# Optimization experiments

Hardware: AMD Instinct MI355X
Metric: run time of the kernel (lower is better)

The kernel has to match this reference:

```python
import jax, jax.numpy as jnp
import numpy as np

B, S, T, E, H = 64, 128, 128, 512, 1024
NEG = -1e9


def setup_inputs() -> dict:
    key = jax.random.key(0)
    ks = jax.random.split(key, 11)
    sc = 0.05
    return {
        "inputs": jax.random.normal(ks[0], (B, T, E), jnp.float32),
        "encoder_hiddens": jax.random.normal(ks[1], (B, S, H), jnp.float32),
        "encoder_finals": jax.random.normal(ks[2], (1, B, H), jnp.float32),
        "src_mask": jnp.ones((B, S), dtype=bool),
        # Bahdanau attention params (torch nn.Linear convention: y = x @ W.T)
        "W_key": jax.random.normal(ks[3], (H, H), jnp.float32) * sc,
        "W_query": jax.random.normal(ks[4], (H, H), jnp.float32) * sc,
        "v_att": jax.random.normal(ks[5], (H,), jnp.float32) * sc,
        # single-layer GRU params, torch gate order (r, z, n)
        "W_ih": jax.random.normal(ks[6], (3 * H, E + H), jnp.float32) * sc,
        "W_hh": jax.random.normal(ks[7], (3 * H, H), jnp.float32) * sc,
        "b_ih": jax.random.normal(ks[8], (3 * H,), jnp.float32) * sc,
        "b_hh": jax.random.normal(ks[9], (3 * H,), jnp.float32) * sc,
    }


def reference(inputs, encoder_hiddens, encoder_finals, src_mask,
              W_key, W_query, v_att, W_ih, W_hh, b_ih, b_hh):
    h_dim = encoder_hiddens.shape[-1]
    # proj_key computed once outside the loop, as in the original
    proj_key = jnp.einsum('bsh,kh->bsk', encoder_hiddens, W_key)  # (B,S,H)

    def step(hidden, x_t):
        # hidden: (1,B,H); x_t: (B,E)
        h = hidden[-1]                                  # (B,H)
        q = h @ W_query.T                               # (B,H)
        e = jnp.tanh(q[:, None, :] + proj_key) @ v_att  # (B,S)
        e = jnp.where(src_mask, e, NEG)
        alphas = jax.nn.softmax(e, axis=-1)
        ctx = jnp.einsum('bs,bsh->bh', alphas, encoder_hiddens)  # (B,H)
        x = jnp.concatenate([x_t, ctx], axis=-1)        # (B,E+H)
        gx = x @ W_ih.T + b_ih                          # (B,3H)
        gh = h @ W_hh.T + b_hh                          # (B,3H)
        r = jax.nn.sigmoid(gx[:, :h_dim] + gh[:, :h_dim])
        z = jax.nn.sigmoid(gx[:, h_dim:2 * h_dim] + gh[:, h_dim:2 * h_dim])
        n = jnp.tanh(gx[:, 2 * h_dim:] + r * gh[:, 2 * h_dim:])
        h_new = (1.0 - z) * n + z * h
        return h_new[None], h_new

    hidden, outs = jax.lax.scan(step, encoder_finals, jnp.swapaxes(inputs, 0, 1))
    outputs = jnp.swapaxes(outs, 0, 1)  # (B,T,H)
    return hidden, outputs
```

## Files before the change

kernel.cpp:

```cpp
#include <hip/hip_runtime.h>
#include <hip/hip_cooperative_groups.h>

namespace cg = cooperative_groups;

#define Bb 64
#define Ss 128
#define Tt 128
#define Ee 512
#define Hh 1024
#define GRID 256
#define NTHR 512
#define GSTRIDE (GRID * NTHR)

using short8 = __attribute__((ext_vector_type(8))) short;
using f32x4  = __attribute__((ext_vector_type(4))) float;
typedef unsigned long long u64;

#define PK_OFF    0u
#define EPART_OFF PK_OFF
#define ENC_OFF   16777216u
#define WQF_OFF   33554432u
#define WHHF_OFF  35651584u
#define WIHF_OFF  41943040u
#define WKF_OFF   51380224u
#define QWS_OFF   53477376u
#define GHWS_OFF  53739520u
#define CTXF_OFF  54525952u
#define HFRG_OFF  54657024u
#define HPRV_OFF  54788096u
#define FLG_OFF   55050240u

__device__ __forceinline__ float fast_tanh(float x) {
  float e = __expf(2.0f * x);
  return 1.0f - __fdividef(2.0f, e + 1.0f);
}
__device__ __forceinline__ float fast_sig(float x) {
  return __fdividef(1.0f, 1.0f + __expf(-x));
}
__device__ __forceinline__ unsigned f2bf(float x) {
  union { float f; unsigned u; } v; v.f = x;
  unsigned r = v.u + 0x7fffu + ((v.u >> 16) & 1u);
  return (r >> 16);
}
__device__ __forceinline__ uint4 pack8(float4 a, float4 b) {
  uint4 u;
  u.x = f2bf(a.x) | (f2bf(a.y) << 16);
  u.y = f2bf(a.z) | (f2bf(a.w) << 16);
  u.z = f2bf(b.x) | (f2bf(b.y) << 16);
  u.w = f2bf(b.z) | (f2bf(b.w) << 16);
  return u;
}
__device__ __forceinline__ void cvt8_store(const float* src, unsigned short* dst) {
  float4 f0 = *(const float4*)src, f1 = *(const float4*)(src + 4);
  *(uint4*)dst = pack8(f0, f1);
}
__device__ __forceinline__ short8 ld_frag(const unsigned short* base, int tile, int lane) {
  return *(const short8*)(base + ((size_t)tile * 64 + lane) * 8);
}
__device__ __forceinline__ short8 cvt8_reg(const float* src) {
  float4 f0 = *(const float4*)src, f1 = *(const float4*)(src + 4);
  union { uint4 u; short8 s; } cv; cv.u = pack8(f0, f1);
  return cv.s;
}

__device__ __forceinline__ u64 ld_coh8(const void* p) {
  return __hip_atomic_load((const u64*)p, __ATOMIC_RELAXED, __HIP_MEMORY_SCOPE_AGENT);
}
__device__ __forceinline__ void st_coh8(void* p, u64 v) {
  __hip_atomic_store((u64*)p, v, __ATOMIC_RELAXED, __HIP_MEMORY_SCOPE_AGENT);
}
__device__ __forceinline__ unsigned ld_coh1(const void* p) {
  return __hip_atomic_load((const unsigned*)p, __ATOMIC_RELAXED, __HIP_MEMORY_SCOPE_AGENT);
}
__device__ __forceinline__ void st_coh1(void* p, unsigned v) {
  __hip_atomic_store((unsigned*)p, v, __ATOMIC_RELAXED, __HIP_MEMORY_SCOPE_AGENT);
}
__device__ __forceinline__ void add_coh1(void* p, unsigned v) {
  __hip_atomic_fetch_add((unsigned*)p, v, __ATOMIC_RELAXED, __HIP_MEMORY_SCOPE_AGENT);
}
__device__ __forceinline__ u64 f2u64(float a, float b) {
  union { float f[2]; u64 u; } c; c.f[0] = a; c.f[1] = b; return c.u;
}
__device__ __forceinline__ float u64lo(u64 v) {
  union { unsigned u; float f; } c; c.u = (unsigned)v; return c.f;
}
__device__ __forceinline__ float u64hi(u64 v) {
  union { unsigned u; float f; } c; c.u = (unsigned)(v >> 32); return c.f;
}

#define ARRIVE_PRE() do { \
  asm volatile("s_waitcnt vmcnt(0)" ::: "memory"); \
  __syncthreads(); } while (0)

template <int K, bool PERM>
__device__ void conv_frag(const float* __restrict__ W, unsigned short* __restrict__ F,
                          int gtid, int total) {
  const int kpg = K / 8;
  for (int i = gtid; i < total; i += GSTRIDE) {
    int np = i / kpg, kg = i - np * kpg;
    int row;
    if (PERM) {
      int ntp = np >> 4, jb = ntp / 3, g = ntp - jb * 3;
      row = g * 1024 + jb * 16 + (np & 15);
    } else row = np;
    int k0 = kg * 8;
    int kt = k0 >> 5, quad = (k0 >> 3) & 3;
    int lane_f = (np & 15) | (quad << 4);
    size_t dst = ((size_t)((np >> 4) * (K / 32) + kt) * 64 + lane_f) * 8;
    cvt8_store(W + (size_t)row * K + k0, F + dst);
  }
}

__global__ void __launch_bounds__(NTHR, 2)
bahdanau_kernel(const float* __restrict__ inputs,
                const float* __restrict__ enc,
                const float* __restrict__ finals,
                const float* __restrict__ Wk,
                const float* __restrict__ Wq,
                const float* __restrict__ vatt,
                const float* __restrict__ Wih,
                const float* __restrict__ Whh,
                const float* __restrict__ bih,
                const float* __restrict__ bhh,
                float* __restrict__ dout,
                char* __restrict__ wsb)
{
  cg::grid_group grid = cg::this_grid();
  __shared__ unsigned short pk_l[128][256];
  __shared__ char scr[40960];

  const int tid  = threadIdx.x;
  const int bid  = blockIdx.x;
  const int lane = tid & 63;
  const int wv   = __builtin_amdgcn_readfirstlane(tid >> 6);
  const int gtid = bid * NTHR + tid;
  const int quad = lane >> 4, col = lane & 15;

  unsigned short* pk   = (unsigned short*)(wsb + PK_OFF);
  float*          epart= (float*)(wsb + EPART_OFF);
  unsigned short* encb = (unsigned short*)(wsb + ENC_OFF);
  unsigned short* wqf  = (unsigned short*)(wsb + WQF_OFF);
  unsigned short* wihf = (unsigned short*)(wsb + WIHF_OFF);
  unsigned short* wkf  = (unsigned short*)(wsb + WKF_OFF);
  float* qws  = (float*)(wsb + QWS_OFF);
  float* ghws = (float*)(wsb + GHWS_OFF);
  unsigned short* ctxf = (unsigned short*)(wsb + CTXF_OFF);
  unsigned short* hfrg = (unsigned short*)(wsb + HFRG_OFF);
  float* hprv = (float*)(wsb + HPRV_OFF);
  unsigned* flags = (unsigned*)(wsb + FLG_OFF);
  unsigned* af = flags;
  unsigned* mb = flags + 8192;
  unsigned* cc = flags + 10240;
  unsigned* hc = flags + 12288;
  unsigned* rc = flags + 13312;
  unsigned* ha = flags + 14336;
  float* hidout = dout;
  float* outs   = dout + Bb * Hh;

  const int batt = bid & 63;
  const int hq   = bid >> 6;

  for (int i = gtid; i < 16384; i += GSTRIDE) flags[i] = 0u;
  for (int i = gtid; i < 1048576; i += GSTRIDE)
    cvt8_store(enc + (size_t)i * 8, encb + (size_t)i * 8);
  conv_frag<1024, false>(Wq,  wqf,  gtid, 131072);
  conv_frag<1024, false>(Wk,  wkf,  gtid, 131072);
  conv_frag<1024, true >(Whh, (unsigned short*)(wsb + WHHF_OFF), gtid, 393216);
  conv_frag<1536, true >(Wih, wihf, gtid, 589824);
  for (int i = gtid; i < 8192; i += GSTRIDE) {
    int b = i >> 7, kg = i & 127, k0 = kg * 8;
    int kt = k0 >> 5, qd = (k0 >> 3) & 3;
    int lf = (b & 15) | (qd << 4);
    cvt8_store(finals + (size_t)b * Hh + k0,
               hfrg + ((size_t)((b >> 4) * 32 + kt) * 64 + lf) * 8);
  }
  for (int i = gtid; i < 16384; i += GSTRIDE)
    ((float4*)hprv)[i] = ((const float4*)finals)[i];
  grid.sync();

  const int wA  = (bid & 7) * 8 + (bid >> 5);
  const int btA = (bid >> 3) & 3;
  const int cgA = wv & 3;
  const int khA = wv >> 2;
  const int ntA = wA * 4 + cgA;
  short8 wAB[16];
  #pragma unroll
  for (int i = 0; i < 16; ++i)
    wAB[i] = ld_frag(wqf, ntA * 32 + khA * 16 + i, lane);

  const int cxC = bid & 7, cmC = bid >> 3;
  const int jbC = cxC * 8 + (cmC >> 2);
  const int bqC = cmC & 3;

  int pqsel;
  {
    int g = lane & 3;
    int wq = hq * 4 + g;
    pqsel = (wq & 7) * 32 + (batt >> 4) * 8 + (wq >> 3);
  }
  int pghsel;
  {
    int wg0 = (64 + 3 * jbC) >> 2, wg1 = (66 + 3 * jbC) >> 2;
    int wg = (lane == 16) ? wg0 : wg1;
    pghsel = (wg & 7) * 32 + bqC * 8 + (wg >> 3);
  }

  float vr2[4];
  {
    float4 vv = *(const float4*)(vatt + hq * 256 + lane * 4);
    vr2[0] = vv.x; vr2[1] = vv.y; vr2[2] = vv.z; vr2[3] = vv.w;
  }

  {
    const int W = bid * 8 + wv;
    const int mt = W >> 2;
    const int ng = W & 3;
    for (int nt2 = 0; nt2 < 16; ++nt2) {
      int nt = ng * 16 + nt2;
      f32x4 acc = {0.f, 0.f, 0.f, 0.f};
      for (int kt = 0; kt < 32; ++kt) {
        short8 a = *(const short8*)(encb + (size_t)(mt * 16 + col) * Hh + kt * 32 + quad * 8);
        short8 b = ld_frag(wkf, nt * 32 + kt, lane);
        acc = __builtin_amdgcn_mfma_f32_16x16x32_bf16(a, b, acc, 0, 0, 0);
      }
      #pragma unroll
      for (int r = 0; r < 4; ++r)
        pk[(size_t)(mt * 16 + quad * 4 + r) * Hh + nt * 16 + col] = (unsigned short)f2bf(acc[r]);
    }
  }
  grid.sync();

  {
    const unsigned short* src = pk + (size_t)batt * Ss * Hh + hq * 256;
    int s = tid >> 2, pq = tid & 3;
    #pragma unroll
    for (int i = 0; i < 8; ++i)
      *(uint4*)&pk_l[s][pq * 64 + i * 8] =
        *(const uint4*)(src + (size_t)s * Hh + pq * 64 + i * 8);
  }
  __syncthreads();

  for (int t = 0; t < Tt; ++t) {
    const unsigned genA = (unsigned)(t + 1);

    __syncthreads();
    if (t > 0 && tid < 64) {
      unsigned tgt = 8u * (unsigned)t;
      for (;;) {
        bool ok = true;
        if (lane < 8) ok = ld_coh1(&hc[(btA * 8 + lane) * 32]) >= tgt;
        if (__all(ok)) break;
        __builtin_amdgcn_s_sleep(2);
      }
    }
    __syncthreads();

    {
      {
        u64* l8 = (u64*)scr;
        const u64* g8 = (const u64*)(hfrg + (size_t)btA * 32 * 64 * 8);
        u64 r[8];
        #pragma unroll
        for (int i = 0; i < 8; ++i) r[i] = ld_coh8(g8 + tid + i * NTHR);
        #pragma unroll
        for (int i = 0; i < 8; ++i) l8[tid + i * NTHR] = r[i];
      }
      __syncthreads();
      if (tid == 0) add_coh1(&ha[(btA * 8 + (wA >> 3)) * 32], 1u);
      const unsigned short* hl = (const unsigned short*)scr;
      f32x4 acc = {0.f, 0.f, 0.f, 0.f};
      #pragma unroll
      for (int i = 0; i < 16; ++i) {
        int kt = khA * 16 + i;
        short8 a = *(const short8*)(hl + ((size_t)kt * 64 + lane) * 8);
        acc = __builtin_amdgcn_mfma_f32_16x16x32_bf16(a, wAB[i], acc, 0, 0, 0);
      }
      __syncthreads();
      float* part = (float*)(scr + 32768);
      #pragma unroll
      for (int r = 0; r < 4; ++r) part[r * 512 + wv * 64 + lane] = acc[r];
      __syncthreads();
      {
        int cg = tid >> 7, rem = tid & 127;
        int qd = rem >> 5, r = (rem >> 3) & 3, clp = rem & 7;
        float v2[2];
        #pragma unroll
        for (int jj = 0; jj < 2; ++jj) {
          int cl = clp * 2 + jj;
          int ln = (qd << 4) | cl;
          v2[jj] = part[r * 512 + cg * 64 + ln]
                 + part[r * 512 + (4 + cg) * 64 + ln];
        }
        int b = btA * 16 + qd * 4 + r;
        int nt_g = wA * 4 + cg;
        if (nt_g < 64)
          st_coh8(&qws[(size_t)b * Hh + nt_g * 16 + clp * 2], f2u64(v2[0], v2[1]));
        else
          st_coh8(&ghws[((size_t)(nt_g - 64) * 64 + b) * 16 + clp * 2], f2u64(v2[0], v2[1]));
      }
    }
    ARRIVE_PRE();
    if (tid == 0) st_coh1(&af[bid * 32], genA);

    if (tid < 64) {
      for (;;) {
        bool ok = true;
        if (lane < 4) ok = ld_coh1(&af[pqsel * 32]) >= genA;
        if (__all(ok)) break;
        __builtin_amdgcn_s_sleep(2);
      }
    }
    __syncthreads();

    {
      float* ep_s = (float*)scr;
      float qr2[4];
      {
        const u64* qb = (const u64*)(qws + (size_t)batt * Hh + hq * 256);
        u64 q01 = ld_coh8(qb + lane * 2), q23 = ld_coh8(qb + lane * 2 + 1);
        qr2[0] = u64lo(q01); qr2[1] = u64hi(q01);
        qr2[2] = u64lo(q23); qr2[3] = u64hi(q23);
      }
      for (int si = 0; si < 16; ++si) {
        int s = wv * 16 + si;
        u64 pkv = *(const u64*)&pk_l[s][lane << 2];
        float pv0 = __uint_as_float(((unsigned)pkv & 0xffffu) << 16);
        float pv1 = __uint_as_float((unsigned)pkv & 0xffff0000u);
        float pv2 = __uint_as_float(((unsigned)(pkv >> 32) & 0xffffu) << 16);
        float pv3 = __uint_as_float((unsigned)(pkv >> 32) & 0xffff0000u);
        float p = vr2[0] * fast_tanh(qr2[0] + pv0);
        p = fmaf(vr2[1], fast_tanh(qr2[1] + pv1), p);
        p = fmaf(vr2[2], fast_tanh(qr2[2] + pv2), p);
        p = fmaf(vr2[3], fast_tanh(qr2[3] + pv3), p);
        #pragma unroll
        for (int m = 1; m < 64; m <<= 1) p += __shfl_xor(p, m, 64);
        if (lane == 0) ep_s[s] = p;
      }
      __syncthreads();
      if (tid < 64) {
        float2 e2 = *(const float2*)&ep_s[tid * 2];
        st_coh8(&epart[((size_t)batt * 4 + hq) * 128 + tid * 2], f2u64(e2.x, e2.y));
      }
    }
    ARRIVE_PRE();
    if (tid == 0) add_coh1(&mb[batt * 32], 1u);
    if (tid == 0) {
      while (ld_coh1(&mb[batt * 32]) < 4u * genA) __builtin_amdgcn_s_sleep(2);
    }
    __syncthreads();

    {
      float* e_s  = (float*)(scr + 512);
      float* al_s = (float*)(scr + 1024);
      float* comb = (float*)(scr + 1536);
      if (tid < 64) {
        float s0 = 0.f, s1 = 0.f;
        #pragma unroll
        for (int k = 0; k < 4; ++k) {
          u64 v = ld_coh8(&epart[((size_t)batt * 4 + k) * 128 + tid * 2]);
          s0 += u64lo(v); s1 += u64hi(v);
        }
        e_s[tid * 2] = s0; e_s[tid * 2 + 1] = s1;
      }
      __syncthreads();
      if (wv == 0) {
        float x0 = e_s[lane], x1 = e_s[lane + 64];
        float m = fmaxf(x0, x1);
        #pragma unroll
        for (int mm = 1; mm < 64; mm <<= 1) m = fmaxf(m, __shfl_xor(m, mm, 64));
        float ex0 = __expf(x0 - m), ex1 = __expf(x1 - m);
        float ssum = ex0 + ex1;
        #pragma unroll
        for (int mm = 1; mm < 64; mm <<= 1) ssum += __shfl_xor(ssum, mm, 64);
        float inv = __fdividef(1.0f, ssum);
        al_s[lane] = ex0 * inv; al_s[lane + 64] = ex1 * inv;
      }
      __syncthreads();
      {
        int tq = tid >> 7, hh = tid & 127;
        float c0 = 0.f, c1 = 0.f;
        const unsigned short* ebase = encb + ((size_t)batt * Ss + tq * 32) * Hh
                                    + hq * 256 + hh * 2;
        #pragma unroll 8
        for (int s2 = 0; s2 < 32; ++s2) {
          float al = al_s[tq * 32 + s2];
          unsigned u = *(const unsigned*)(ebase + (size_t)s2 * Hh);
          c0 = fmaf(al, __uint_as_float((u & 0xffffu) << 16), c0);
          c1 = fmaf(al, __uint_as_float(u & 0xffff0000u), c1);
        }
        comb[(tq * 128 + hh) * 2 + 0] = c0;
        comb[(tq * 128 + hh) * 2 + 1] = c1;
      }
      __syncthreads();
      if (tid < 64) {
        unsigned tgt = 8u * (unsigned)t;
        for (;;) {
          bool ok = true;
          if (lane < 8) ok = ld_coh1(&rc[((batt >> 4) * 8 + lane) * 32]) >= tgt;
          if (__all(ok)) break;
          __builtin_amdgcn_s_sleep(2);
        }
      }
      __syncthreads();
      if (tid < 128) {
        float c0 = comb[tid * 2] + comb[(128 + tid) * 2]
                 + comb[(256 + tid) * 2] + comb[(384 + tid) * 2];
        float c1 = comb[tid * 2 + 1] + comb[(128 + tid) * 2 + 1]
                 + comb[(256 + tid) * 2 + 1] + comb[(384 + tid) * 2 + 1];
        int h = hq * 256 + tid * 2;
        int kt = h >> 5, qd = (h >> 3) & 3, elem = h & 7;
        int lf = (batt & 15) | (qd << 4);
        unsigned hw = f2bf(c0) | (f2bf(c1) << 16);
        st_coh1(ctxf + ((size_t)((batt >> 4) * 32 + kt) * 64 + lf) * 8 + elem, hw);
      }
    }
    ARRIVE_PRE();
    if (tid == 0) add_coh1(&cc[batt * 32], 1u);

    if (tid < 64) {
      for (;;) {
        bool ok = true;
        if (lane < 16) ok = ld_coh1(&cc[(bqC * 16 + lane) * 32]) >= 4u * genA;
        else if (lane < 18) ok = ld_coh1(&af[pghsel * 32]) >= genA;
        if (__all(ok)) break;
        __builtin_amdgcn_s_sleep(2);
      }
    }
    __syncthreads();

    {
      const int jb = jbC;
      const int bq = bqC;
      {
        u64* l8 = (u64*)scr;
        const u64* g8 = (const u64*)(ctxf + (size_t)bq * 32 * 64 * 8);
        u64 r[8];
        #pragma unroll
        for (int i = 0; i < 8; ++i) r[i] = ld_coh8(g8 + tid + i * NTHR);
        #pragma unroll
        for (int i = 0; i < 8; ++i) l8[tid + i * NTHR] = r[i];
      }
      __syncthreads();
      if (tid == 0) add_coh1(&rc[(bqC * 8 + (jbC >> 3)) * 32], 1u);
      float* gxl = (float*)(scr + 32768);
      if (wv < 6) {
        const int g  = wv >> 1;
        const int kh = wv & 1;
        const int ntp = jb * 3 + g;
        const unsigned short* lctx = (const unsigned short*)scr;
        f32x4 acc = {0.f, 0.f, 0.f, 0.f};
        for (int k2 = 0; k2 < 24; ++k2) {
          int kt = kh * 24 + k2;
          short8 a;
          if (kt < 16) {
            int brow = bq * 16 + col;
            a = cvt8_reg(inputs + ((size_t)brow * Tt + t) * Ee + kt * 32 + quad * 8);
          } else {
            a = *(const short8*)(lctx + ((size_t)(kt - 16) * 64 + lane) * 8);
          }
          short8 bfr = ld_frag(wihf, ntp * 48 + kt, lane);
          acc = __builtin_amdgcn_mfma_f32_16x16x32_bf16(a, bfr, acc, 0, 0, 0);
        }
        #pragma unroll
        for (int r = 0; r < 4; ++r) gxl[r * 384 + wv * 64 + lane] = acc[r];
      }
      __syncthreads();
      if (tid < 64) {
        unsigned tgt = 8u * genA;
        for (;;) {
          bool ok = true;
          if (lane < 8) ok = ld_coh1(&ha[(bqC * 8 + lane) * 32]) >= tgt;
          if (__all(ok)) break;
          __builtin_amdgcn_s_sleep(2);
        }
      }
      __syncthreads();
      if (tid < 128) {
        int bloc = tid >> 3, jp = tid & 7;
        int b = bq * 16 + bloc;
        int j0p = jb * 16 + jp * 2;
        int qd = bloc >> 2, r = bloc & 3;
        u64 g0 = ld_coh8(&ghws[((size_t)(jb * 3 + 0) * 64 + b) * 16 + jp * 2]);
        u64 g1 = ld_coh8(&ghws[((size_t)(jb * 3 + 1) * 64 + b) * 16 + jp * 2]);
        u64 g2 = ld_coh8(&ghws[((size_t)(jb * 3 + 2) * 64 + b) * 16 + jp * 2]);
        u64 hpu = ld_coh8(&hprv[(size_t)b * Hh + j0p]);
        float hn2[2];
        #pragma unroll
        for (int jj = 0; jj < 2; ++jj) {
          int j = j0p + jj;
          int cl = jp * 2 + jj;
          int ll = (qd << 4) | cl;
          float gx0 = gxl[r * 384 + 0 * 64 + ll] + gxl[r * 384 + 1 * 64 + ll];
          float gx1 = gxl[r * 384 + 2 * 64 + ll] + gxl[r * 384 + 3 * 64 + ll];
          float gx2 = gxl[r * 384 + 4 * 64 + ll] + gxl[r * 384 + 5 * 64 + ll];
          float gh0 = jj ? u64hi(g0) : u64lo(g0);
          float gh1 = jj ? u64hi(g1) : u64lo(g1);
          float gh2 = jj ? u64hi(g2) : u64lo(g2);
          float hp  = jj ? u64hi(hpu) : u64lo(hpu);
          float rr = fast_sig(gx0 + bih[0 * 1024 + j] + gh0 + bhh[0 * 1024 + j]);
          float zz = fast_sig(gx1 + bih[1 * 1024 + j] + gh1 + bhh[1 * 1024 + j]);
          float nn = fast_tanh(gx2 + bih[2 * 1024 + j] + rr * (gh2 + bhh[2 * 1024 + j]));
          hn2[jj] = (1.0f - zz) * nn + zz * hp;
        }
        *(float2*)(outs + ((size_t)b * Tt + t) * Hh + j0p) = make_float2(hn2[0], hn2[1]);
        st_coh8(&hprv[(size_t)b * Hh + j0p], f2u64(hn2[0], hn2[1]));
        int kt = j0p >> 5, qd2 = (j0p >> 3) & 3;
        int lfh = (b & 15) | (qd2 << 4);
        unsigned hw = f2bf(hn2[0]) | (f2bf(hn2[1]) << 16);
        st_coh1(hfrg + ((size_t)(bq * 32 + kt) * 64 + lfh) * 8 + (j0p & 7), hw);
      }
    }
    ARRIVE_PRE();
    if (tid == 0) add_coh1(&hc[(bqC * 8 + (jbC >> 3)) * 32], 1u);
  }

  grid.sync();
  {
    int idx = gtid;
    if (idx < Bb * Hh) {
      unsigned u = ld_coh1(&hprv[idx]);
      hidout[idx] = __uint_as_float(u);
    }
  }
}

extern "C" void kernel_launch(void* const* d_in, const int* in_sizes, int n_in,
                              void* d_out, int out_size, void* d_ws, size_t ws_size,
                              hipStream_t stream) {
  const float* inputs = (const float*)d_in[0];
  const float* enc    = (const float*)d_in[1];
  const float* finals = (const float*)d_in[2];
  const float* Wk  = (const float*)d_in[4];
  const float* Wq  = (const float*)d_in[5];
  const float* v   = (const float*)d_in[6];
  const float* Wih = (const float*)d_in[7];
  const float* Whh = (const float*)d_in[8];
  const float* bih = (const float*)d_in[9];
  const float* bhh = (const float*)d_in[10];
  float* out = (float*)d_out;
  char* ws   = (char*)d_ws;

  void* args[] = {(void*)&inputs, (void*)&enc, (void*)&finals, (void*)&Wk,
                  (void*)&Wq, (void*)&v, (void*)&Wih, (void*)&Whh,
                  (void*)&bih, (void*)&bhh, (void*)&out, (void*)&ws};
  (void)hipLaunchCooperativeKernel((const void*)bahdanau_kernel,
                                   dim3(GRID), dim3(NTHR), args, 0, stream);
}
```

Measured before the change: 4.201 ms.

## Overlap input-projection GEMM with context wait and prefetch GRU operands

Splits the phase-C wait so the block first waits only for the gh flags, then prefetches gh and previous-hidden values and computes the x_t part of the input projection before waiting on the context counters. The x part (kt<16) now runs on the kh==0 waves while the attention/context of other blocks finishes, so it leaves the critical path. GRU biases are hoisted into registers once before the time loop. Work across waves becomes less balanced (kh==0 waves do 24 k-steps versus 24 for kh==1, with part of that done earlier), and a few more registers stay live across the loop.

```diff
diff --git a/kernel.cpp b/kernel.cpp
--- a/kernel.cpp
+++ b/kernel.cpp
@@ -198,17 +198,31 @@
     int wq = hq * 4 + g;
     pqsel = (wq & 7) * 32 + (batt >> 4) * 8 + (wq >> 3);
   }
-  int pghsel;
+  int pghsel2;
   {
     int wg0 = (64 + 3 * jbC) >> 2, wg1 = (66 + 3 * jbC) >> 2;
-    int wg = (lane == 16) ? wg0 : wg1;
-    pghsel = (wg & 7) * 32 + bqC * 8 + (wg >> 3);
+    int wgx = (lane & 1) ? wg1 : wg0;
+    pghsel2 = (wgx & 7) * 32 + bqC * 8 + (wgx >> 3);
   }
 
   float vr2[4];
   {
     float4 vv = *(const float4*)(vatt + hq * 256 + lane * 4);
     vr2[0] = vv.x; vr2[1] = vv.y; vr2[2] = vv.z; vr2[3] = vv.w;
+  }
+
+  const int blocC = tid >> 3, jpC = tid & 7;
+  const int bC    = bqC * 16 + blocC;
+  const int j0pC  = jbC * 16 + jpC * 2;
+  float2 bi0v = {0,0}, bi1v = {0,0}, bi2v = {0,0};
+  float2 bh0v = {0,0}, bh1v = {0,0}, bh2v = {0,0};
+  if (tid < 128) {
+    bi0v = *(const float2*)&bih[0 * 1024 + j0pC];
+    bi1v = *(const float2*)&bih[1 * 1024 + j0pC];
+    bi2v = *(const float2*)&bih[2 * 1024 + j0pC];
+    bh0v = *(const float2*)&bhh[0 * 1024 + j0pC];
+    bh1v = *(const float2*)&bhh[1 * 1024 + j0pC];
+    bh2v = *(const float2*)&bhh[2 * 1024 + j0pC];
   }
 
   {
@@ -417,20 +431,46 @@
     ARRIVE_PRE();
     if (tid == 0) add_coh1(&cc[batt * 32], 1u);
 
-    if (tid < 64) {
-      for (;;) {
-        bool ok = true;
-        if (lane < 16) ok = ld_coh1(&cc[(bqC * 16 + lane) * 32]) >= 4u * genA;
-        else if (lane < 18) ok = ld_coh1(&af[pghsel * 32]) >= genA;
-        if (__all(ok)) break;
-        __builtin_amdgcn_s_sleep(2);
-      }
-    }
-    __syncthreads();
-
     {
       const int jb = jbC;
       const int bq = bqC;
+      const int g  = wv >> 1;
+      const int kh = wv & 1;
+      const int ntp = jb * 3 + g;
+      if (tid < 64) {
+        for (;;) {
+          bool ok = true;
+          if (lane < 2) ok = ld_coh1(&af[pghsel2 * 32]) >= genA;
+          if (__all(ok)) break;
+          __builtin_amdgcn_s_sleep(2);
+        }
+      }
+      __syncthreads();
+      u64 g0 = 0, g1 = 0, g2 = 0, hpu = 0;
+      if (tid < 128) {
+        g0 = ld_coh8(&ghws[((size_t)(jb * 3 + 0) * 64 + bC) * 16 + jpC * 2]);
+        g1 = ld_coh8(&ghws[((size_t)(jb * 3 + 1) * 64 + bC) * 16 + jpC * 2]);
+        g2 = ld_coh8(&ghws[((size_t)(jb * 3 + 2) * 64 + bC) * 16 + jpC * 2]);
+        hpu = ld_coh8(&hprv[(size_t)bC * Hh + j0pC]);
+      }
+      f32x4 accC = {0.f, 0.f, 0.f, 0.f};
+      if (wv < 6 && kh == 0) {
+        for (int kt = 0; kt < 16; ++kt) {
+          int brow = bq * 16 + col;
+          short8 a = cvt8_reg(inputs + ((size_t)brow * Tt + t) * Ee + kt * 32 + quad * 8);
+          short8 bfr = ld_frag(wihf, ntp * 48 + kt, lane);
+          accC = __builtin_amdgcn_mfma_f32_16x16x32_bf16(a, bfr, accC, 0, 0, 0);
+        }
+      }
+      if (tid < 64) {
+        for (;;) {
+          bool ok = true;
+          if (lane < 16) ok = ld_coh1(&cc[(bqC * 16 + lane) * 32]) >= 4u * genA;
+          if (__all(ok)) break;
+          __builtin_amdgcn_s_sleep(2);
+        }
+      }
+      __syncthreads();
       {
         u64* l8 = (u64*)scr;
         const u64* g8 = (const u64*)(ctxf + (size_t)bq * 32 * 64 * 8);
@@ -444,25 +484,16 @@
       if (tid == 0) add_coh1(&rc[(bqC * 8 + (jbC >> 3)) * 32], 1u);
       float* gxl = (float*)(scr + 32768);
       if (wv < 6) {
-        const int g  = wv >> 1;
-        const int kh = wv & 1;
-        const int ntp = jb * 3 + g;
         const unsigned short* lctx = (const unsigned short*)scr;
-        f32x4 acc = {0.f, 0.f, 0.f, 0.f};
-        for (int k2 = 0; k2 < 24; ++k2) {
-          int kt = kh * 24 + k2;
-          short8 a;
-          if (kt < 16) {
-            int brow = bq * 16 + col;
-            a = cvt8_reg(inputs + ((size_t)brow * Tt + t) * Ee + kt * 32 + quad * 8);
-          } else {
-            a = *(const short8*)(lctx + ((size_t)(kt - 16) * 64 + lane) * 8);
-          }
+        int kt0 = kh ? 24 : 16;
+        int kt1 = kh ? 48 : 24;
+        for (int kt = kt0; kt < kt1; ++kt) {
+          short8 a = *(const short8*)(lctx + ((size_t)(kt - 16) * 64 + lane) * 8);
           short8 bfr = ld_frag(wihf, ntp * 48 + kt, lane);
-          acc = __builtin_amdgcn_mfma_f32_16x16x32_bf16(a, bfr, acc, 0, 0, 0);
-        }
-        #pragma unroll
-        for (int r = 0; r < 4; ++r) gxl[r * 384 + wv * 64 + lane] = acc[r];
+          accC = __builtin_amdgcn_mfma_f32_16x16x32_bf16(a, bfr, accC, 0, 0, 0);
+        }
+        #pragma unroll
+        for (int r = 0; r < 4; ++r) gxl[r * 384 + wv * 64 + lane] = accC[r];
       }
       __syncthreads();
       if (tid < 64) {
@@ -476,19 +507,11 @@
       }
       __syncthreads();
       if (tid < 128) {
-        int bloc = tid >> 3, jp = tid & 7;
-        int b = bq * 16 + bloc;
-        int j0p = jb * 16 + jp * 2;
-        int qd = bloc >> 2, r = bloc & 3;
-        u64 g0 = ld_coh8(&ghws[((size_t)(jb * 3 + 0) * 64 + b) * 16 + jp * 2]);
-        u64 g1 = ld_coh8(&ghws[((size_t)(jb * 3 + 1) * 64 + b) * 16 + jp * 2]);
-        u64 g2 = ld_coh8(&ghws[((size_t)(jb * 3 + 2) * 64 + b) * 16 + jp * 2]);
-        u64 hpu = ld_coh8(&hprv[(size_t)b * Hh + j0p]);
+        int qd = blocC >> 2, r = blocC & 3;
         float hn2[2];
         #pragma unroll
         for (int jj = 0; jj < 2; ++jj) {
-          int j = j0p + jj;
-          int cl = jp * 2 + jj;
+          int cl = jpC * 2 + jj;
           int ll = (qd << 4) | cl;
           float gx0 = gxl[r * 384 + 0 * 64 + ll] + gxl[r * 384 + 1 * 64 + ll];
           float gx1 = gxl[r * 384 + 2 * 64 + ll] + gxl[r * 384 + 3 * 64 + ll];
@@ -497,17 +520,23 @@
           float gh1 = jj ? u64hi(g1) : u64lo(g1);
           float gh2 = jj ? u64hi(g2) : u64lo(g2);
           float hp  = jj ? u64hi(hpu) : u64lo(hpu);
-          float rr = fast_sig(gx0 + bih[0 * 1024 + j] + gh0 + bhh[0 * 1024 + j]);
-          float zz = fast_sig(gx1 + bih[1 * 1024 + j] + gh1 + bhh[1 * 1024 + j]);
-          float nn = fast_tanh(gx2 + bih[2 * 1024 + j] + rr * (gh2 + bhh[2 * 1024 + j]));
+          float bi0 = jj ? bi0v.y : bi0v.x;
+          float bi1 = jj ? bi1v.y : bi1v.x;
+          float bi2 = jj ? bi2v.y : bi2v.x;
+          float bh0 = jj ? bh0v.y : bh0v.x;
+          float bh1 = jj ? bh1v.y : bh1v.x;
+          float bh2 = jj ? bh2v.y : bh2v.x;
+          float rr = fast_sig(gx0 + bi0 + gh0 + bh0);
+          float zz = fast_sig(gx1 + bi1 + gh1 + bh1);
+          float nn = fast_tanh(gx2 + bi2 + rr * (gh2 + bh2));
           hn2[jj] = (1.0f - zz) * nn + zz * hp;
         }
-        *(float2*)(outs + ((size_t)b * Tt + t) * Hh + j0p) = make_float2(hn2[0], hn2[1]);
-        st_coh8(&hprv[(size_t)b * Hh + j0p], f2u64(hn2[0], hn2[1]));
-        int kt = j0p >> 5, qd2 = (j0p >> 3) & 3;
-        int lfh = (b & 15) | (qd2 << 4);
+        *(float2*)(outs + ((size_t)bC * Tt + t) * Hh + j0pC) = make_float2(hn2[0], hn2[1]);
+        st_coh8(&hprv[(size_t)bC * Hh + j0pC], f2u64(hn2[0], hn2[1]));
+        int kt = j0pC >> 5, qd2 = (j0pC >> 3) & 3;
+        int lfh = (bC & 15) | (qd2 << 4);
         unsigned hw = f2bf(hn2[0]) | (f2bf(hn2[1]) << 16);
-        st_coh1(hfrg + ((size_t)(bq * 32 + kt) * 64 + lfh) * 8 + (j0p & 7), hw);
+        st_coh1(hfrg + ((size_t)(bqC * 32 + kt) * 64 + lfh) * 8 + (j0pC & 7), hw);
       }
     }
     ARRIVE_PRE();
```

After: 3.866 ms. 1.09x faster.
